# Kernel tuning notes

Hardware: AMD Instinct MI355X
Metric: run time of the kernel (lower is better)

The kernel has to match this reference:

```python
import jax, jax.numpy as jnp
import numpy as np

D_G, D_2D, D_3D = 512, 768, 1024
D_F, RANK, ATTN_H = 256, 16, 512
B = 8192


def _xavier(key, shape):
    fan_out, fan_in = shape
    lim = float(np.sqrt(6.0 / (fan_in + fan_out)))
    return jax.random.uniform(key, shape, jnp.float32, -lim, lim)


def setup_inputs() -> dict:
    key = jax.random.key(0)
    ks = jax.random.split(key, 12)
    inp = {
        "h_g": jax.random.normal(ks[0], (B, D_G), jnp.float32),
        "h_2d": jax.random.normal(ks[1], (B, D_2D), jnp.float32),
        "h_3d": jax.random.normal(ks[2], (B, D_3D), jnp.float32),
        # modality projections (torch Linear: y = x @ W.T + b)
        "Wg": _xavier(ks[3], (D_F, D_G)),   "bg": jnp.zeros((D_F,), jnp.float32),
        "W2": _xavier(ks[4], (D_F, D_2D)),  "b2": jnp.zeros((D_F,), jnp.float32),
        "W3": _xavier(ks[5], (D_F, D_3D)),  "b3": jnp.zeros((D_F,), jnp.float32),
        # LayerNorm affine params
        "ln_g_w": jnp.ones((D_F,), jnp.float32),  "ln_g_b": jnp.zeros((D_F,), jnp.float32),
        "ln_2_w": jnp.ones((D_F,), jnp.float32),  "ln_2_b": jnp.zeros((D_F,), jnp.float32),
        "ln_3_w": jnp.ones((D_F,), jnp.float32),  "ln_3_b": jnp.zeros((D_F,), jnp.float32),
        # rank expansions (no bias)
        "U": _xavier(ks[6], (RANK * D_F, D_F)),
        "V": _xavier(ks[7], (RANK * D_F, D_F)),
        "S": _xavier(ks[8], (RANK * D_F, D_F)),
        # attention MLP
        "Wa1": _xavier(ks[9], (ATTN_H, D_G + D_2D + D_3D)), "ba1": jnp.zeros((ATTN_H,), jnp.float32),
        "Wa2": _xavier(ks[10], (RANK, ATTN_H)),             "ba2": jnp.zeros((RANK,), jnp.float32),
    }
    return inp


def _layernorm(x, w, b, eps=1e-5):
    mu = jnp.mean(x, axis=-1, keepdims=True)
    var = jnp.var(x, axis=-1, keepdims=True)
    return (x - mu) * jax.lax.rsqrt(var + eps) * w + b


def reference(h_g, h_2d, h_3d, Wg, bg, W2, b2, W3, b3,
              ln_g_w, ln_g_b, ln_2_w, ln_2_b, ln_3_w, ln_3_b,
              U, V, S, Wa1, ba1, Wa2, ba2):
    # proj + LN + ReLU (dropout=0 / eval mode)
    g = jax.nn.relu(_layernorm(h_g @ Wg.T + bg, ln_g_w, ln_g_b))
    d2 = jax.nn.relu(_layernorm(h_2d @ W2.T + b2, ln_2_w, ln_2_b))
    d3 = jax.nn.relu(_layernorm(h_3d @ W3.T + b3, ln_3_w, ln_3_b))
    b = g.shape[0]
    # rank expansion: (B, R, d_f)
    g_r = (g @ U.T).reshape(b, RANK, D_F)
    d2_r = (d2 @ V.T).reshape(b, RANK, D_F)
    d3_r = (d3 @ S.T).reshape(b, RANK, D_F)
    z_r = g_r * d2_r * d3_r  # elementwise tri-linear product
    # rank attention from raw modality concat
    h_cat = jnp.concatenate([h_g, h_2d, h_3d], axis=-1)
    beta = jax.nn.softmax(jax.nn.relu(h_cat @ Wa1.T + ba1) @ Wa2.T + ba2, axis=-1)  # (B, R)
    z = jnp.einsum('brd,br->bd', z_r, beta)  # (B, d_f)
    return z
```

## Files before the change

kernel.cpp:

```cpp
#include <hip/hip_runtime.h>
#include <stdint.h>

#define B_ROWS 8192
#define DG 512
#define D2 768
#define D3 1024
#define DCAT 2304
#define DF 256
#define RANK 16
#define AH 512

#define OFF_WG 0
#define OFF_W2 131072
#define OFF_W3 327680
#define OFF_U  589824
#define OFF_V  1638400
#define OFF_S  2686976
#define OFF_WA1 3735552

#define WS_WBUF  0u
#define WS_HG    9830400u
#define WS_H2    18219008u
#define WS_H3    30801920u
#define WS_GBUF  9830400u
#define WS_PROJ  47579136u
#define WS_A1P   72744960u
#define WS_BETA  89522176u
#define WS_ZPART 47579136u
#define WS_REQUIRED 94240768u

typedef __attribute__((ext_vector_type(8))) short short8;
typedef __attribute__((ext_vector_type(4))) float f32x4;

__device__ inline unsigned short f2bf(float f) {
  union { float f; unsigned int u; } v; v.f = f;
  unsigned int u = v.u + 0x7fffu + ((v.u >> 16) & 1u);
  return (unsigned short)(u >> 16);
}
__device__ inline float bf2f(unsigned short h) {
  union { float f; unsigned int u; } v; v.u = ((unsigned int)h) << 16;
  return v.f;
}

typedef const unsigned int __attribute__((address_space(1)))* as1_u32p;
typedef unsigned int __attribute__((address_space(3)))* as3_u32p;

__device__ inline void g2l16(const unsigned short* g, unsigned short* l) {
  __builtin_amdgcn_global_load_lds((as1_u32p)g, (as3_u32p)l, 16, 0, 0);
}


__global__ __launch_bounds__(256) void cvt_split_k(const float* __restrict__ hg,
                                                   const float* __restrict__ h2,
                                                   const float* __restrict__ h3,
                                                   const float* __restrict__ Wg,
                                                   const float* __restrict__ W2,
                                                   const float* __restrict__ W3,
                                                   const float* __restrict__ U,
                                                   const float* __restrict__ V,
                                                   const float* __restrict__ S,
                                                   const float* __restrict__ Wa1,
                                                   unsigned short* __restrict__ hgb,
                                                   unsigned short* __restrict__ h2b,
                                                   unsigned short* __restrict__ h3b,
                                                   unsigned short* __restrict__ wbuf) {
  const int bid = blockIdx.x;
  const float* src;
  unsigned short* dst;
  int e;
  if (bid < 18432) {
    e = (bid * 256 + threadIdx.x) * 4;
    if (e < 4194304)        { src = hg + e;            dst = hgb + e; }
    else if (e < 10485760)  { src = h2 + (e - 4194304); dst = h2b + (e - 4194304); }
    else                    { src = h3 + (e - 10485760); dst = h3b + (e - 10485760); }
  } else {
    e = ((bid - 18432) * 256 + threadIdx.x) * 4;
    dst = wbuf + e;
    if (e < OFF_W2)       src = Wg  + e;
    else if (e < OFF_W3)  src = W2  + (e - OFF_W2);
    else if (e < OFF_U)   src = W3  + (e - OFF_W3);
    else if (e < OFF_V)   src = U   + (e - OFF_U);
    else if (e < OFF_S)   src = V   + (e - OFF_V);
    else if (e < OFF_WA1) src = S   + (e - OFF_S);
    else                  src = Wa1 + (e - OFF_WA1);
  }
  float4 v = *(const float4*)src;
  ushort4 o;
  o.x = f2bf(v.x); o.y = f2bf(v.y); o.z = f2bf(v.z); o.w = f2bf(v.w);
  *(ushort4*)dst = o;
}


__device__ __forceinline__ void gemm_mainloop_acc(const unsigned short* Ag, int lda,
                                                  const unsigned short* Bg, int ldb,
                                                  int K,
                                                  unsigned short* lA, unsigned short* lB,
                                                  f32x4 acc[4][4]) {
  const int tid = threadIdx.x;
  const int lane = tid & 63;
  const int wr = tid >> 7;
  const int wc = (tid >> 6) & 1;
  const int row_s = tid >> 3;
  const int kc_s = (((tid & 7) ^ ((tid >> 3) & 7)) << 3);
  const int mbase = wr * 64 + (lane & 15);
  const int nbase = wc * 64 + (lane & 15);
  const int kq = lane >> 4;
  const int h = lane & 7;

  const int nsteps = K >> 6;
  for (int ks = 0; ks < nsteps; ++ks) {
    const int k0 = ks << 6;
    __syncthreads();
#pragma unroll
    for (int p = 0; p < 4; ++p) {
      const int row = p * 32 + row_s;
      const int lofs = (p * 256 + tid) * 8;
      g2l16(Ag + (size_t)row * lda + k0 + kc_s, lA + lofs);
      g2l16(Bg + (size_t)row * ldb + k0 + kc_s, lB + lofs);
    }
    __syncthreads();
#pragma unroll
    for (int kk = 0; kk < 2; ++kk) {
      const int kch = (kk << 2) + kq;
      const int ko = ((kch ^ h) << 3);
      short8 af[4], bfr[4];
#pragma unroll
      for (int t = 0; t < 4; ++t) {
        af[t]  = *(const short8*)(lA + (mbase + t * 16) * 64 + ko);
        bfr[t] = *(const short8*)(lB + (nbase + t * 16) * 64 + ko);
      }
#pragma unroll
      for (int ti = 0; ti < 4; ++ti)
#pragma unroll
        for (int tj = 0; tj < 4; ++tj)
          acc[ti][tj] = __builtin_amdgcn_mfma_f32_16x16x32_bf16(af[ti], bfr[tj], acc[ti][tj], 0, 0, 0);
    }
  }
}

__device__ __forceinline__ void zero_acc(f32x4 acc[4][4]) {
#pragma unroll
  for (int i = 0; i < 4; ++i)
#pragma unroll
    for (int j = 0; j < 4; ++j)
      acc[i][j] = (f32x4){0.f, 0.f, 0.f, 0.f};
}


__global__ __launch_bounds__(256) void fatgemm_k(const unsigned short* __restrict__ hgb,
                                                 const unsigned short* __restrict__ h2b,
                                                 const unsigned short* __restrict__ h3b,
                                                 const unsigned short* __restrict__ wbuf,
                                                 float* __restrict__ proj,
                                                 unsigned short* __restrict__ a1part) {
  __shared__ __align__(16) unsigned short lA[128 * 64];
  __shared__ __align__(16) unsigned short lB[128 * 64];
  const int bid = blockIdx.x;
  f32x4 acc[4][4];
  const int lane = threadIdx.x & 63;
  const int wr = threadIdx.x >> 7, wc = (threadIdx.x >> 6) & 1;
  zero_acc(acc);

  if (bid < 512) {
    const int half = bid >> 8;
    const int local = bid & 255;
    const int m0 = (local >> 2) << 7;
    const int n0 = (local & 3) << 7;
    const unsigned short* Bb = wbuf + OFF_WA1 + (size_t)n0 * DCAT;
    if (half == 0) {
      gemm_mainloop_acc(hgb + (size_t)m0 * DG, DG, Bb, DCAT, DG, lA, lB, acc);
      gemm_mainloop_acc(h2b + (size_t)m0 * D2, D2, Bb + DG, DCAT, D2, lA, lB, acc);
    } else {
      gemm_mainloop_acc(h3b + (size_t)m0 * D3, D3, Bb + DG + D2, DCAT, D3, lA, lB, acc);
    }
    unsigned short* out = a1part + (size_t)half * (B_ROWS * AH);
    const int r0 = m0 + wr * 64 + ((lane >> 4) << 2);
    const int c0 = n0 + wc * 64 + (lane & 15);
#pragma unroll
    for (int ti = 0; ti < 4; ++ti)
#pragma unroll
      for (int tj = 0; tj < 4; ++tj)
#pragma unroll
        for (int i = 0; i < 4; ++i)
          out[(size_t)(r0 + ti * 16 + i) * AH + (c0 + tj * 16)] = f2bf(acc[ti][tj][i]);
  } else {
    const int b = bid - 512;
    const int z = b >> 7;
    const int local = b & 127;
    const int m0 = (local >> 1) << 7;
    const int n0 = (local & 1) << 7;
    const int Kz   = (z == 0) ? DG : (z == 1 ? D2 : D3);
    const unsigned short* Ab = (z == 0) ? hgb : (z == 1 ? h2b : h3b);
    const int woff = (z == 0) ? OFF_WG : (z == 1 ? OFF_W2 : OFF_W3);
    gemm_mainloop_acc(Ab + (size_t)m0 * Kz, Kz,
                      wbuf + woff + (size_t)n0 * Kz, Kz, Kz, lA, lB, acc);
    float* out = proj + (size_t)z * B_ROWS * DF;
    const int r0 = m0 + wr * 64 + ((lane >> 4) << 2);
    const int c0 = n0 + wc * 64 + (lane & 15);
#pragma unroll
    for (int ti = 0; ti < 4; ++ti)
#pragma unroll
      for (int tj = 0; tj < 4; ++tj)
#pragma unroll
        for (int i = 0; i < 4; ++i)
          out[(size_t)(r0 + ti * 16 + i) * DF + (c0 + tj * 16)] = acc[ti][tj][i];
  }
}


__global__ __launch_bounds__(256) void rank_fused_k(const unsigned short* __restrict__ gbuf,
                                                    const unsigned short* __restrict__ wbuf,
                                                    const float* __restrict__ beta,
                                                    float* __restrict__ zpart) {
  __shared__ __align__(16) unsigned short lA[2 * 128 * 128];
  __shared__ __align__(16) unsigned short lB[2 * 128 * 128];
  __shared__ float lbeta[4 * 128];
  const int m0 = blockIdx.x * 128;
  const int d0 = blockIdx.y * 128;
  const int rg = blockIdx.z * 4;
  const int tid = threadIdx.x;

  for (int i = tid; i < 512; i += 256) {
    const int rr = i >> 7, row = i & 127;
    lbeta[i] = beta[(size_t)(m0 + row) * RANK + rg + rr];
  }

  const int lane = tid & 63;
  const int wr = tid >> 7, wc = (tid >> 6) & 1;
  const int row_s = tid >> 4;
  const int kc_s = (((tid & 15) ^ ((tid >> 4) & 15)) << 3);
  const int mbase = wr * 64 + (lane & 15);
  const int nbase = wc * 64 + (lane & 15);
  const int kq = lane >> 4;
  const int h = lane & 15;
  const int lr0 = wr * 64 + ((lane >> 4) << 2);

  auto stage = [&](int rr, int zi, int ks, unsigned short* dA, unsigned short* dB) {
    const unsigned short* Ag = gbuf + (size_t)zi * (B_ROWS * DF) + (size_t)m0 * DF + (ks << 7);
    const unsigned short* Bg = wbuf + OFF_U + (size_t)zi * 1048576
                             + (size_t)((rg + rr) * 256 + d0) * DF + (ks << 7);
#pragma unroll
    for (int q = 0; q < 8; ++q) {
      const int row = q * 16 + row_s;
      const int lofs = (q * 256 + tid) * 8;
      g2l16(Ag + (size_t)row * DF + kc_s, dA + lofs);
      g2l16(Bg + (size_t)row * DF + kc_s, dB + lofs);
    }
  };

  f32x4 zacc[4][4], prod[4][4], acc[4][4];
#pragma unroll
  for (int ti = 0; ti < 4; ++ti)
#pragma unroll
    for (int tj = 0; tj < 4; ++tj) {
      zacc[ti][tj] = (f32x4){0.f, 0.f, 0.f, 0.f};
      acc[ti][tj]  = (f32x4){0.f, 0.f, 0.f, 0.f};
    }

  auto compute = [&](const unsigned short* sA, const unsigned short* sB) {
#pragma unroll
    for (int kk = 0; kk < 4; ++kk) {
      const int kch = (kk << 2) + kq;
      const int ko = ((kch ^ h) << 3);
      short8 af[4], bfr[4];
#pragma unroll
      for (int t = 0; t < 4; ++t) {
        af[t]  = *(const short8*)(sA + (mbase + t * 16) * 128 + ko);
        bfr[t] = *(const short8*)(sB + (nbase + t * 16) * 128 + ko);
      }
#pragma unroll
      for (int ti = 0; ti < 4; ++ti)
#pragma unroll
        for (int tj = 0; tj < 4; ++tj)
          acc[ti][tj] = __builtin_amdgcn_mfma_f32_16x16x32_bf16(af[ti], bfr[tj], acc[ti][tj], 0, 0, 0);
    }
  };

  stage(0, 0, 0, lA, lB);
  for (int p = 0; p < 12; ++p) {
    const int rr = p / 3;
    const int zi = p - rr * 3;
    __syncthreads();
    stage(rr, zi, 1, lA + 16384, lB + 16384);
    compute(lA, lB);
    __syncthreads();
    if (p + 1 < 12) {
      const int pn = p + 1;
      const int rrn = pn / 3;
      stage(rrn, pn - rrn * 3, 0, lA, lB);
    }
    compute(lA + 16384, lB + 16384);

    if (zi == 0) {
#pragma unroll
      for (int ti = 0; ti < 4; ++ti)
#pragma unroll
        for (int tj = 0; tj < 4; ++tj)
          prod[ti][tj] = acc[ti][tj];
    } else if (zi == 1) {
#pragma unroll
      for (int ti = 0; ti < 4; ++ti)
#pragma unroll
        for (int tj = 0; tj < 4; ++tj)
          prod[ti][tj] *= acc[ti][tj];
    } else {
#pragma unroll
      for (int ti = 0; ti < 4; ++ti) {
        const float4 b4 = *(const float4*)(lbeta + rr * 128 + lr0 + ti * 16);
        const float bv[4] = {b4.x, b4.y, b4.z, b4.w};
#pragma unroll
        for (int tj = 0; tj < 4; ++tj)
#pragma unroll
          for (int i = 0; i < 4; ++i)
            zacc[ti][tj][i] += prod[ti][tj][i] * acc[ti][tj][i] * bv[i];
      }
    }
#pragma unroll
    for (int ti = 0; ti < 4; ++ti)
#pragma unroll
      for (int tj = 0; tj < 4; ++tj)
        acc[ti][tj] = (f32x4){0.f, 0.f, 0.f, 0.f};
  }

  float* zp = zpart + (size_t)blockIdx.z * (B_ROWS * DF);
  const int c0 = d0 + wc * 64 + (lane & 15);
#pragma unroll
  for (int ti = 0; ti < 4; ++ti)
#pragma unroll
    for (int tj = 0; tj < 4; ++tj)
#pragma unroll
      for (int i = 0; i < 4; ++i)
        zp[(size_t)(m0 + lr0 + ti * 16 + i) * DF + (c0 + tj * 16)] = zacc[ti][tj][i];
}


__global__ __launch_bounds__(256) void zsum_k(const float* __restrict__ zpart,
                                              float* __restrict__ z) {
  const int idx = blockIdx.x * 256 + threadIdx.x;
  const size_t e = (size_t)idx * 4;
  const size_t stride = (size_t)B_ROWS * DF;
  float4 a = *(const float4*)(zpart + e);
  float4 b = *(const float4*)(zpart + stride + e);
  float4 c = *(const float4*)(zpart + 2 * stride + e);
  float4 d = *(const float4*)(zpart + 3 * stride + e);
  float4 o;
  o.x = (a.x + b.x) + (c.x + d.x);
  o.y = (a.y + b.y) + (c.y + d.y);
  o.z = (a.z + b.z) + (c.z + d.z);
  o.w = (a.w + b.w) + (c.w + d.w);
  *(float4*)(z + e) = o;
}


__global__ __launch_bounds__(256) void post_k(const float* __restrict__ proj,
                                              const float* __restrict__ bg, const float* __restrict__ b2, const float* __restrict__ b3,
                                              const float* __restrict__ wg, const float* __restrict__ wbg,
                                              const float* __restrict__ w2, const float* __restrict__ wb2,
                                              const float* __restrict__ w3, const float* __restrict__ wb3,
                                              unsigned short* __restrict__ gout,
                                              const unsigned short* __restrict__ a1part,
                                              const float* __restrict__ ba1,
                                              const float* __restrict__ Wa2,
                                              const float* __restrict__ ba2,
                                              float* __restrict__ beta) {
  const int bid = blockIdx.x;
  if (bid < 6144) {
    const int gid = bid * 4 + (threadIdx.x >> 6);
    const int lane = threadIdx.x & 63;
    const int z = gid >> 13;
    const int row = gid & (B_ROWS - 1);
    const float* bias = z == 0 ? bg : (z == 1 ? b2 : b3);
    const float* lw = z == 0 ? wg : (z == 1 ? w2 : w3);
    const float* lb = z == 0 ? wbg : (z == 1 ? wb2 : wb3);
    const float* x = proj + (size_t)z * B_ROWS * DF + (size_t)row * DF + lane * 4;
    float4 v = *(const float4*)x;
    float4 bb = *(const float4*)(bias + lane * 4);
    v.x += bb.x; v.y += bb.y; v.z += bb.z; v.w += bb.w;
    float s = v.x + v.y + v.z + v.w;
    float q = v.x * v.x + v.y * v.y + v.z * v.z + v.w * v.w;
#pragma unroll
    for (int m = 1; m < 64; m <<= 1) { s += __shfl_xor(s, m, 64); q += __shfl_xor(q, m, 64); }
    const float mean = s * (1.f / DF);
    const float var = q * (1.f / DF) - mean * mean;
    const float rs = rsqrtf(var + 1e-5f);
    float4 w4 = *(const float4*)(lw + lane * 4);
    float4 b4 = *(const float4*)(lb + lane * 4);
    ushort4 o;
    o.x = f2bf(fmaxf((v.x - mean) * rs * w4.x + b4.x, 0.f));
    o.y = f2bf(fmaxf((v.y - mean) * rs * w4.y + b4.y, 0.f));
    o.z = f2bf(fmaxf((v.z - mean) * rs * w4.z + b4.z, 0.f));
    o.w = f2bf(fmaxf((v.w - mean) * rs * w4.w + b4.w, 0.f));
    *(ushort4*)(gout + (size_t)z * B_ROWS * DF + (size_t)row * DF + lane * 4) = o;
  } else {
    __shared__ float lw[RANK * AH];
    for (int i = threadIdx.x; i < RANK * AH / 4; i += 256)
      *(float4*)(lw + i * 4) = *(const float4*)(Wa2 + i * 4);
    __syncthreads();
    const int row = (bid - 6144) * 4 + (threadIdx.x >> 6);
    const int lane = threadIdx.x & 63;
    const unsigned short* h0 = a1part + (size_t)row * AH + lane * 8;
    const unsigned short* h1 = h0 + (size_t)B_ROWS * AH;
    const uint4 p0 = *(const uint4*)h0;
    const uint4 p1 = *(const uint4*)h1;
    const unsigned int u0[4] = {p0.x, p0.y, p0.z, p0.w};
    const unsigned int u1[4] = {p1.x, p1.y, p1.z, p1.w};
    float4 ca = *(const float4*)(ba1 + lane * 8);
    float4 cb = *(const float4*)(ba1 + lane * 8 + 4);
    const float bias[8] = {ca.x, ca.y, ca.z, ca.w, cb.x, cb.y, cb.z, cb.w};
    float av[8];
#pragma unroll
    for (int j = 0; j < 4; ++j) {
      const float s0 = bf2f((unsigned short)(u0[j] & 0xffffu)) + bf2f((unsigned short)(u1[j] & 0xffffu));
      const float s1 = bf2f((unsigned short)(u0[j] >> 16)) + bf2f((unsigned short)(u1[j] >> 16));
      av[2 * j]     = fmaxf(s0 + bias[2 * j], 0.f);
      av[2 * j + 1] = fmaxf(s1 + bias[2 * j + 1], 0.f);
    }
    float lg[RANK];
#pragma unroll
    for (int r = 0; r < RANK; ++r) {
      const float* wrow = lw + r * AH + lane * 8;
      float4 wa = *(const float4*)wrow;
      float4 wb = *(const float4*)(wrow + 4);
      float p = av[0] * wa.x + av[1] * wa.y + av[2] * wa.z + av[3] * wa.w
              + av[4] * wb.x + av[5] * wb.y + av[6] * wb.z + av[7] * wb.w;
#pragma unroll
      for (int m = 1; m < 64; m <<= 1) p += __shfl_xor(p, m, 64);
      lg[r] = p + ba2[r];
    }
    float mx = lg[0];
#pragma unroll
    for (int r = 1; r < RANK; ++r) mx = fmaxf(mx, lg[r]);
    float den = 0.f;
#pragma unroll
    for (int r = 0; r < RANK; ++r) { lg[r] = __expf(lg[r] - mx); den += lg[r]; }
    const float inv = 1.f / den;
    if (lane < RANK) {
      float mine = 0.f;
#pragma unroll
      for (int r = 0; r < RANK; ++r) mine = (lane == r) ? lg[r] : mine;
      beta[(size_t)row * RANK + lane] = mine * inv;
    }
  }
}


extern "C" void kernel_launch(void* const* d_in, const int* in_sizes, int n_in,
                              void* d_out, int out_size, void* d_ws, size_t ws_size,
                              hipStream_t stream) {
  if (ws_size < (size_t)WS_REQUIRED) return;

  const float* h_g   = (const float*)d_in[0];
  const float* h_2d  = (const float*)d_in[1];
  const float* h_3d  = (const float*)d_in[2];
  const float* Wg    = (const float*)d_in[3];
  const float* bg    = (const float*)d_in[4];
  const float* W2    = (const float*)d_in[5];
  const float* b2    = (const float*)d_in[6];
  const float* W3    = (const float*)d_in[7];
  const float* b3    = (const float*)d_in[8];
  const float* ln_g_w = (const float*)d_in[9];
  const float* ln_g_b = (const float*)d_in[10];
  const float* ln_2_w = (const float*)d_in[11];
  const float* ln_2_b = (const float*)d_in[12];
  const float* ln_3_w = (const float*)d_in[13];
  const float* ln_3_b = (const float*)d_in[14];
  const float* U     = (const float*)d_in[15];
  const float* V     = (const float*)d_in[16];
  const float* S     = (const float*)d_in[17];
  const float* Wa1   = (const float*)d_in[18];
  const float* ba1   = (const float*)d_in[19];
  const float* Wa2   = (const float*)d_in[20];
  const float* ba2   = (const float*)d_in[21];

  char* ws = (char*)d_ws;
  unsigned short* wbuf   = (unsigned short*)(ws + WS_WBUF);
  unsigned short* hgb    = (unsigned short*)(ws + WS_HG);
  unsigned short* h2b    = (unsigned short*)(ws + WS_H2);
  unsigned short* h3b    = (unsigned short*)(ws + WS_H3);
  unsigned short* gbuf   = (unsigned short*)(ws + WS_GBUF);
  float*          proj   = (float*)(ws + WS_PROJ);
  unsigned short* a1part = (unsigned short*)(ws + WS_A1P);
  float*          beta   = (float*)(ws + WS_BETA);
  float*          zpart  = (float*)(ws + WS_ZPART);
  float* z = (float*)d_out;

  cvt_split_k<<<dim3(23232), dim3(256), 0, stream>>>(h_g, h_2d, h_3d,
                                                     Wg, W2, W3, U, V, S, Wa1,
                                                     hgb, h2b, h3b, wbuf);
  fatgemm_k<<<dim3(896), dim3(256), 0, stream>>>(hgb, h2b, h3b, wbuf, proj, a1part);
  post_k<<<dim3(8192), dim3(256), 0, stream>>>(proj, bg, b2, b3, ln_g_w, ln_g_b,
                                               ln_2_w, ln_2_b, ln_3_w, ln_3_b, gbuf,
                                               a1part, ba1, Wa2, ba2, beta);
  rank_fused_k<<<dim3(64, 2, 4), dim3(256), 0, stream>>>(gbuf, wbuf, beta, zpart);
  zsum_k<<<dim3(2048), dim3(256), 0, stream>>>(zpart, z);
}
```

Measured before the change: 322.2 us.

## Shrink rank GEMM K-tile to 64 and pipeline loads with explicit vmcnt waits

Halves the LDS K-tile in the fused rank-expansion kernel from 128 to 64 and keeps two stages in flight, so each step issues the next stage's global-to-LDS loads before waiting on the current one with an explicit s_waitcnt vmcnt instead of a full __syncthreads. It cuts LDS per block so two blocks can fit per CU (launch_bounds 256,2), and raises wave priority around the MFMA burst. The risks are tighter register limits from the occupancy hint, possible spills, and correctness depending on the hand-counted vmcnt values matching the number of outstanding loads.

```diff
diff --git a/kernel.cpp b/kernel.cpp
--- a/kernel.cpp
+++ b/kernel.cpp
@@ -208,12 +208,12 @@
 }
 
 
-__global__ __launch_bounds__(256) void rank_fused_k(const unsigned short* __restrict__ gbuf,
-                                                    const unsigned short* __restrict__ wbuf,
-                                                    const float* __restrict__ beta,
-                                                    float* __restrict__ zpart) {
-  __shared__ __align__(16) unsigned short lA[2 * 128 * 128];
-  __shared__ __align__(16) unsigned short lB[2 * 128 * 128];
+__global__ __launch_bounds__(256, 2) void rank_fused_k(const unsigned short* __restrict__ gbuf,
+                                                       const unsigned short* __restrict__ wbuf,
+                                                       const float* __restrict__ beta,
+                                                       float* __restrict__ zpart) {
+  __shared__ __align__(16) unsigned short lA[2 * 128 * 64];
+  __shared__ __align__(16) unsigned short lB[2 * 128 * 64];
   __shared__ float lbeta[4 * 128];
   const int m0 = blockIdx.x * 128;
   const int d0 = blockIdx.y * 128;
@@ -224,27 +224,32 @@
     const int rr = i >> 7, row = i & 127;
     lbeta[i] = beta[(size_t)(m0 + row) * RANK + rg + rr];
   }
+  __syncthreads();
 
   const int lane = tid & 63;
   const int wr = tid >> 7, wc = (tid >> 6) & 1;
-  const int row_s = tid >> 4;
-  const int kc_s = (((tid & 15) ^ ((tid >> 4) & 15)) << 3);
+  const int row_s = tid >> 3;
+  const int kc_s = (((tid & 7) ^ ((tid >> 3) & 7)) << 3);
   const int mbase = wr * 64 + (lane & 15);
   const int nbase = wc * 64 + (lane & 15);
   const int kq = lane >> 4;
-  const int h = lane & 15;
+  const int h = lane & 7;
   const int lr0 = wr * 64 + ((lane >> 4) << 2);
 
-  auto stage = [&](int rr, int zi, int ks, unsigned short* dA, unsigned short* dB) {
-    const unsigned short* Ag = gbuf + (size_t)zi * (B_ROWS * DF) + (size_t)m0 * DF + (ks << 7);
-    const unsigned short* Bg = wbuf + OFF_U + (size_t)zi * 1048576
-                             + (size_t)((rg + rr) * 256 + d0) * DF + (ks << 7);
-#pragma unroll
-    for (int q = 0; q < 8; ++q) {
-      const int row = q * 16 + row_s;
+  const unsigned short* Abase = gbuf + (size_t)(m0 + row_s) * DF + kc_s;
+  const unsigned short* Bbase = wbuf + OFF_U + (size_t)(rg * 256 + d0 + row_s) * DF + kc_s;
+
+  auto stage = [&](int t, unsigned short* dA, unsigned short* dB) {
+    const int p = t >> 2, ks = t & 3;
+    const int rr = p / 3;
+    const int zi = p - rr * 3;
+    const unsigned short* Ag = Abase + (size_t)zi * (B_ROWS * DF) + ks * 64;
+    const unsigned short* Bg = Bbase + (size_t)zi * 1048576 + (size_t)rr * (256 * DF) + ks * 64;
+#pragma unroll
+    for (int q = 0; q < 4; ++q) {
       const int lofs = (q * 256 + tid) * 8;
-      g2l16(Ag + (size_t)row * DF + kc_s, dA + lofs);
-      g2l16(Bg + (size_t)row * DF + kc_s, dB + lofs);
+      g2l16(Ag + (size_t)q * 32 * DF, dA + lofs);
+      g2l16(Bg + (size_t)q * 32 * DF, dB + lofs);
     }
   };
 
@@ -259,37 +264,46 @@
 
   auto compute = [&](const unsigned short* sA, const unsigned short* sB) {
 #pragma unroll
-    for (int kk = 0; kk < 4; ++kk) {
+    for (int kk = 0; kk < 2; ++kk) {
       const int kch = (kk << 2) + kq;
       const int ko = ((kch ^ h) << 3);
       short8 af[4], bfr[4];
 #pragma unroll
-      for (int t = 0; t < 4; ++t) {
-        af[t]  = *(const short8*)(sA + (mbase + t * 16) * 128 + ko);
-        bfr[t] = *(const short8*)(sB + (nbase + t * 16) * 128 + ko);
+      for (int t4 = 0; t4 < 4; ++t4) {
+        af[t4]  = *(const short8*)(sA + (mbase + t4 * 16) * 64 + ko);
+        bfr[t4] = *(const short8*)(sB + (nbase + t4 * 16) * 64 + ko);
       }
+      __builtin_amdgcn_s_setprio(1);
 #pragma unroll
       for (int ti = 0; ti < 4; ++ti)
 #pragma unroll
         for (int tj = 0; tj < 4; ++tj)
           acc[ti][tj] = __builtin_amdgcn_mfma_f32_16x16x32_bf16(af[ti], bfr[tj], acc[ti][tj], 0, 0, 0);
+      __builtin_amdgcn_s_setprio(0);
     }
   };
 
-  stage(0, 0, 0, lA, lB);
+  stage(0, lA, lB);
+  stage(1, lA + 8192, lB + 8192);
+
   for (int p = 0; p < 12; ++p) {
     const int rr = p / 3;
     const int zi = p - rr * 3;
-    __syncthreads();
-    stage(rr, zi, 1, lA + 16384, lB + 16384);
-    compute(lA, lB);
-    __syncthreads();
-    if (p + 1 < 12) {
-      const int pn = p + 1;
-      const int rrn = pn / 3;
-      stage(rrn, pn - rrn * 3, 0, lA, lB);
-    }
-    compute(lA + 16384, lB + 16384);
+#pragma unroll
+    for (int ks = 0; ks < 4; ++ks) {
+      const int t = (p << 2) + ks;
+      const int b = t & 1;
+      unsigned short* cA = lA + b * 8192;
+      unsigned short* cB = lB + b * 8192;
+      if (t < 47) asm volatile("s_waitcnt vmcnt(8)" ::: "memory");
+      else        asm volatile("s_waitcnt vmcnt(0)" ::: "memory");
+      __builtin_amdgcn_s_barrier();
+      __builtin_amdgcn_sched_barrier(0);
+      compute(cA, cB);
+      __builtin_amdgcn_sched_barrier(0);
+      __builtin_amdgcn_s_barrier();
+      if (t + 2 < 48) stage(t + 2, cA, cB);
+    }
 
     if (zi == 0) {
 #pragma unroll
```

Measured after the change: 303.4 us. -5.8%, faster.
